# Performance work log

Measured on AMD Instinct MI355X. Metric: run time of the kernel, lower is better.

Reference implementation:

```python
import math
import jax, jax.numpy as jnp
import numpy as np

EPS = 1e-5

def _ln(x, g, b, axes):
    # LayerNormalization4D / 4DCF: mean/var (unbiased=False) over `axes`
    mu = x.mean(axis=axes, keepdims=True)
    var = ((x - mu) ** 2).mean(axis=axes, keepdims=True)
    return (x - mu) / jnp.sqrt(var + EPS) * g + b

def _prelu(x, a):
    return jnp.where(x >= 0, x, a * x)

def _unfold(x, ks, hs):
    # x: [N, C, Q] -> [N, L, C*ks]; patch layout (c, k) matches F.unfold
    N, C, Qd = x.shape
    L = (Qd - ks) // hs + 1
    idx = jnp.arange(L) * hs
    p = x[:, :, idx[:, None] + jnp.arange(ks)]  # [N, C, L, ks]
    return p.transpose(0, 2, 1, 3).reshape(N, L, C * ks)

def _lstm_dir(xs, Wi, Wh, bi, bh, H):
    # xs: [N, L, Cin]; torch gate order i, f, g, o
    xg = jnp.einsum('nlc,gc->nlg', xs, Wi) + bi + bh  # [N, L, 4H]
    def step(carry, gt):
        h, c = carry
        g = gt + h @ Wh.T
        i, f, gg, o = jnp.split(g, 4, axis=-1)
        c = jax.nn.sigmoid(f) * c + jax.nn.sigmoid(i) * jnp.tanh(gg)
        h = jax.nn.sigmoid(o) * jnp.tanh(c)
        return (h, c), h
    N = xs.shape[0]
    z = jnp.zeros((N, H), xs.dtype)
    _, hs = jax.lax.scan(step, (z, z), jnp.swapaxes(xg, 0, 1))
    return jnp.swapaxes(hs, 0, 1)

def _bilstm(x, wih, whh, bih, bhh):
    H = whh.shape[-1]
    f = _lstm_dir(x, wih[0], whh[0], bih[0], bhh[0], H)
    bk = _lstm_dir(x[:, ::-1], wih[1], whh[1], bih[1], bhh[1], H)[:, ::-1]
    return jnp.concatenate([f, bk], axis=-1)

def _convT1d(x, w, b):
    # x: [N, I, L]; w: [I, O, K] (torch ConvTranspose1d layout); stride 1
    K = w.shape[2]
    w2 = jnp.transpose(w, (1, 0, 2))[:, :, ::-1]
    y = jax.lax.conv_general_dilated(x, w2, (1,), [(K - 1, K - 1)],
                                     dimension_numbers=('NCH', 'OIH', 'NCH'))
    return y + b[None, :, None]

def _forward(x, mouth, intra_g, intra_b, intra_wih, intra_whh, intra_bih, intra_bhh,
             intra_lw, intra_lb, inter_g, inter_b, inter_wih, inter_whh, inter_bih,
             inter_bhh, inter_lw, inter_lb, qw, qb, qa, qg, qbe, kw, kb, ka, kg, kbe,
             vw, vb, va, vg, vbe, pw, pb, pa, pg, pbe):
    emb_ks, emb_hs = 4, 1
    B, C, oT, oQ = x.shape
    T = math.ceil((oT - emb_ks) / emb_hs) * emb_hs + emb_ks
    Qd = math.ceil((oQ - emb_ks) / emb_hs) * emb_hs + emb_ks
    x = jnp.pad(x, ((0, 0), (0, 0), (0, T - oT), (0, Qd - oQ)))
    inp = x
    # ---- intra (biLSTM along freq axis) ----
    h = _ln(inp, intra_g[None, :, None, None], intra_b[None, :, None, None], (1,))
    h = h.transpose(0, 2, 1, 3).reshape(B * T, C, Qd)
    h = _unfold(h, emb_ks, emb_hs)                          # [B*T, L, C*ks]
    h = _bilstm(h, intra_wih, intra_whh, intra_bih, intra_bhh)
    h = _convT1d(h.transpose(0, 2, 1), intra_lw, intra_lb)  # [B*T, C, Qd]
    intra = h.reshape(B, T, C, Qd).transpose(0, 2, 1, 3) + inp
    # ---- inter (biLSTM along time axis) ----
    h = _ln(intra, inter_g[None, :, None, None], inter_b[None, :, None, None], (1,))
    h = h.transpose(0, 3, 1, 2).reshape(B * Qd, C, T)
    h = _unfold(h, emb_ks, emb_hs)
    h = _bilstm(h, inter_wih, inter_whh, inter_bih, inter_bhh)
    h = _convT1d(h.transpose(0, 2, 1), inter_lw, inter_lb)  # [B*Qd, C, T]
    inter = h.reshape(B, Qd, C, T).transpose(0, 2, 3, 1) + intra
    inter = inter[..., :oT, :oQ]                             # [B, C, oT, oQ]
    # ---- multi-head full self-attention over time (conv1x1 QKV per head) ----
    NH = qw.shape[0]
    def qkv(w, b_, a_, g_, be_):
        y = jnp.einsum('bctf,hec->hbetf', inter, w) + b_[:, None, :, None, None]
        y = _prelu(y, a_[:, None, None, None, None])
        return _ln(y, g_[:, None, :, None, :], be_[:, None, :, None, :], (2, 4))
    Qh = qkv(qw, qb, qa, qg, qbe)   # [H, B, E, T, F]
    Kh = qkv(kw, kb, ka, kg, kbe)
    Vh = qkv(vw, vb, va, vg, vbe)   # [H, B, D, T, F]
    E = Qh.shape[2]; D = Vh.shape[2]; F = oQ
    q2 = Qh.transpose(0, 1, 3, 2, 4).reshape(NH, B, oT, E * F)
    k2 = Kh.transpose(0, 1, 3, 2, 4).reshape(NH, B, oT, E * F)
    v2 = Vh.transpose(0, 1, 3, 2, 4).reshape(NH, B, oT, D * F)
    scale = 1.0 / jnp.sqrt(jnp.asarray(E * F, x.dtype))
    attn = jax.nn.softmax(jnp.einsum('hbte,hbse->hbts', q2, k2) * scale, axis=-1)
    o = jnp.einsum('hbts,hbsd->hbtd', attn, v2).reshape(NH, B, oT, D, F)
    o = o.transpose(1, 0, 3, 2, 4).reshape(B, NH * D, oT, F)
    # ---- concat projection ----
    p = jnp.einsum('bctf,oc->botf', o, pw) + pb[None, :, None, None]
    p = _prelu(p, pa)
    p = _ln(p, pg[None, :, None, :], pbe[None, :, None, :], (1, 3))
    return p + inter

def setup_inputs() -> dict:
    key = jax.random.key(0)
    keys = iter(jax.random.split(key, 48))
    f32 = jnp.float32
    def nrm(shape, s=0.05):
        return jax.random.normal(next(keys), shape, f32) * s
    B, C, T, F = 2, 48, 512, 65
    K, H, NH, E = 4, 192, 4, 8
    Cin = C * K
    D = C // NH
    return {
        'x': jax.random.normal(next(keys), (B, C, T, F), f32),
        'mouth': jax.random.normal(next(keys), (B, 64), f32),
        'intra_g': jnp.ones((C,), f32), 'intra_b': jnp.zeros((C,), f32),
        'intra_wih': nrm((2, 4 * H, Cin)), 'intra_whh': nrm((2, 4 * H, H)),
        'intra_bih': nrm((2, 4 * H)), 'intra_bhh': nrm((2, 4 * H)),
        'intra_lw': nrm((2 * H, C, K)), 'intra_lb': nrm((C,)),
        'inter_g': jnp.ones((C,), f32), 'inter_b': jnp.zeros((C,), f32),
        'inter_wih': nrm((2, 4 * H, Cin)), 'inter_whh': nrm((2, 4 * H, H)),
        'inter_bih': nrm((2, 4 * H)), 'inter_bhh': nrm((2, 4 * H)),
        'inter_lw': nrm((2 * H, C, K)), 'inter_lb': nrm((C,)),
        'qw': nrm((NH, E, C)), 'qb': nrm((NH, E)), 'qa': 0.25 * jnp.ones((NH,), f32),
        'qg': jnp.ones((NH, E, F), f32), 'qbe': jnp.zeros((NH, E, F), f32),
        'kw': nrm((NH, E, C)), 'kb': nrm((NH, E)), 'ka': 0.25 * jnp.ones((NH,), f32),
        'kg': jnp.ones((NH, E, F), f32), 'kbe': jnp.zeros((NH, E, F), f32),
        'vw': nrm((NH, D, C)), 'vb': nrm((NH, D)), 'va': 0.25 * jnp.ones((NH,), f32),
        'vg': jnp.ones((NH, D, F), f32), 'vbe': jnp.zeros((NH, D, F), f32),
        'pw': nrm((C, C)), 'pb': nrm((C,)), 'pa': jnp.float32(0.25),
        'pg': jnp.ones((C, F), f32), 'pbe': jnp.zeros((C, F), f32),
    }

def reference(x, mouth, intra_g, intra_b, intra_wih, intra_whh, intra_bih, intra_bhh,
              intra_lw, intra_lb, inter_g, inter_b, inter_wih, inter_whh, inter_bih,
              inter_bhh, inter_lw, inter_lb, qw, qb, qa, qg, qbe, kw, kb, ka, kg, kbe,
              vw, vb, va, vg, vbe, pw, pb, pa, pg, pbe):
    return _forward(x, mouth, intra_g, intra_b, intra_wih, intra_whh, intra_bih,
                    intra_bhh, intra_lw, intra_lb, inter_g, inter_b, inter_wih,
                    inter_whh, inter_bih, inter_bhh, inter_lw, inter_lb, qw, qb, qa,
                    qg, qbe, kw, kb, ka, kg, kbe, vw, vb, va, vg, vbe, pw, pb, pa,
                    pg, pbe)
```

## Files before the change

### kernel.cpp

```cpp
#include <hip/hip_runtime.h>
#include <hip/hip_bf16.h>

typedef __bf16 bf16x8 __attribute__((ext_vector_type(8)));
typedef unsigned short u16x8 __attribute__((ext_vector_type(8)));
typedef float f32x4 __attribute__((ext_vector_type(4)));

#define DEV static __device__ __forceinline__

DEV unsigned short f2bf(float f){
  __hip_bfloat16 h = __float2bfloat16(f);
  return __builtin_bit_cast(unsigned short, h);
}
DEV float b2f(unsigned short u){
  return __bfloat162float(__builtin_bit_cast(__hip_bfloat16, u));
}
DEV float sig2(float xs){
  return __builtin_amdgcn_rcpf(1.0f + __builtin_amdgcn_exp2f(-xs));
}
DEV float tanh2s(float xs){
  return 1.0f - 2.0f*__builtin_amdgcn_rcpf(__builtin_amdgcn_exp2f(xs + xs) + 1.0f);
}
DEV float tanh_n(float x){
  return 1.0f - 2.0f*__builtin_amdgcn_rcpf(__builtin_amdgcn_exp2f(x * 2.885390082f) + 1.0f);
}
DEV void lds_barrier(){
  asm volatile("s_waitcnt lgkmcnt(0)\ns_barrier" ::: "memory");
}


__global__ void zero16(uint4* p, size_t n){
  size_t i = (size_t)blockIdx.x*blockDim.x + threadIdx.x;
  size_t st = (size_t)gridDim.x*blockDim.x;
  uint4 z = make_uint4(0u,0u,0u,0u);
  for (; i < n; i += st) p[i] = z;
}

__global__ void zero_pads(unsigned short* hs, int NSEQ, int Qrows, int L){
  int i = blockIdx.x*256 + threadIdx.x;
  int total = NSEQ*6*384;
  if (i < total){
    int t = i/(6*384); int rem = i - t*(6*384);
    int r = rem/384, c = rem - r*384;
    int row = r < 3 ? r : L + r;
    hs[((size_t)t*Qrows + row)*384 + c] = 0;
  }
}

__global__ void cast_bf(const float* __restrict__ s, unsigned short* __restrict__ d, int n, float scale){
  int i = blockIdx.x*256 + threadIdx.x;
  if (i < n) d[i] = f2bf(s[i]*scale);
}

__global__ void cast_wi(const float* __restrict__ s, unsigned short* __restrict__ d, float scale){
  int i = blockIdx.x*256 + threadIdx.x;
  if (i < 294912){
    int dn = i/192, k = i - dn*192;
    int c = k >> 2, kk = k & 3;
    d[(size_t)dn*192 + kk*48 + c] = f2bf(s[i]*scale);
  }
}

__global__ void bias_comb(const float* __restrict__ a, const float* __restrict__ b,
                          float* __restrict__ d, int n, float scale){
  int i = blockIdx.x*256 + threadIdx.x;
  if (i < n) d[i] = (a[i] + b[i])*scale;
}

__global__ void lwt_build(const float* __restrict__ lw, unsigned short* __restrict__ lwt){
  int i = blockIdx.x*256 + threadIdx.x;
  if (i < 384*48*4){
    int m = i / 192; int rest = i - m*192; int c = rest >> 2; int k = rest & 3;
    lwt[(size_t)c*1536 + k*384 + m] = f2bf(lw[i]);
  }
}

__global__ __launch_bounds__(256) void ln_unf_intra(
    const float* __restrict__ in, const float* __restrict__ g,
    const float* __restrict__ be, unsigned short* __restrict__ unf)
{
  int bt = blockIdx.x; int b = bt >> 9, t = bt & 511;
  __shared__ float v[48][66];
  __shared__ float mu[65], rs[65];
  __shared__ float g_l[48], b_l[48];
  const float* base = in + (size_t)b*(48*512*65) + (size_t)t*65;
  for (int i = threadIdx.x; i < 48*65; i += 256){
    int c = i/65, q = i - c*65;
    v[c][q] = base[(size_t)c*(512*65) + q];
  }
  if (threadIdx.x < 48){ g_l[threadIdx.x] = g[threadIdx.x]; b_l[threadIdx.x] = be[threadIdx.x]; }
  __syncthreads();
  if (threadIdx.x < 65){
    int q = threadIdx.x; float s=0.f, s2=0.f;
    #pragma unroll
    for (int c = 0; c < 48; c++){ float x = v[c][q]; s += x; s2 += x*x; }
    float m = s*(1.0f/48.0f);
    mu[q] = m; rs[q] = rsqrtf(s2*(1.0f/48.0f) - m*m + 1e-5f);
  }
  __syncthreads();
  unsigned short* orow = unf + (size_t)(b*512 + t)*62*192;
  for (int idx = threadIdx.x; idx < 62*24; idx += 256){
    int l = idx/24, jg = idx - l*24;
    int kk = jg/6, c0 = (jg - kk*6)*8;
    int q = l + kk;
    ushort4 p0, p1;
    float mq = mu[q], rq = rs[q];
    p0.x = f2bf((v[c0+0][q]-mq)*rq*g_l[c0+0] + b_l[c0+0]);
    p0.y = f2bf((v[c0+1][q]-mq)*rq*g_l[c0+1] + b_l[c0+1]);
    p0.z = f2bf((v[c0+2][q]-mq)*rq*g_l[c0+2] + b_l[c0+2]);
    p0.w = f2bf((v[c0+3][q]-mq)*rq*g_l[c0+3] + b_l[c0+3]);
    p1.x = f2bf((v[c0+4][q]-mq)*rq*g_l[c0+4] + b_l[c0+4]);
    p1.y = f2bf((v[c0+5][q]-mq)*rq*g_l[c0+5] + b_l[c0+5]);
    p1.z = f2bf((v[c0+6][q]-mq)*rq*g_l[c0+6] + b_l[c0+6]);
    p1.w = f2bf((v[c0+7][q]-mq)*rq*g_l[c0+7] + b_l[c0+7]);
    *(ushort4*)(orow + (size_t)l*192 + kk*48 + c0) = p0;
    *(ushort4*)(orow + (size_t)l*192 + kk*48 + c0 + 4) = p1;
  }
}

__global__ __launch_bounds__(256) void ln_unf_inter(
    const float* __restrict__ in, const float* __restrict__ g,
    const float* __restrict__ be, unsigned short* __restrict__ unf)
{
  int bt = blockIdx.x; int b = bt >> 9, t = bt & 511;
  __shared__ float v[48][66];
  __shared__ float mu[65], rs[65];
  __shared__ float g_l[48], b_l[48];
  const float* base = in + (size_t)b*(48*512*65) + (size_t)t*65;
  for (int i = threadIdx.x; i < 48*65; i += 256){
    int c = i/65, q = i - c*65;
    v[c][q] = base[(size_t)c*(512*65) + q];
  }
  if (threadIdx.x < 48){ g_l[threadIdx.x] = g[threadIdx.x]; b_l[threadIdx.x] = be[threadIdx.x]; }
  __syncthreads();
  if (threadIdx.x < 65){
    int q = threadIdx.x; float s=0.f, s2=0.f;
    #pragma unroll
    for (int c = 0; c < 48; c++){ float x = v[c][q]; s += x; s2 += x*x; }
    float m = s*(1.0f/48.0f);
    mu[q] = m; rs[q] = rsqrtf(s2*(1.0f/48.0f) - m*m + 1e-5f);
  }
  __syncthreads();
  for (int idx = threadIdx.x; idx < 4*65*6; idx += 256){
    int s = idx/390;
    int rem = idx - s*390;
    int q = rem/6, c0 = (rem - q*6)*8;
    int l = t - 3 + s, kk = 3 - s;
    if (l < 0 || l > 508) continue;
    float mq = mu[q], rq = rs[q];
    ushort4 p0, p1;
    p0.x = f2bf((v[c0+0][q]-mq)*rq*g_l[c0+0] + b_l[c0+0]);
    p0.y = f2bf((v[c0+1][q]-mq)*rq*g_l[c0+1] + b_l[c0+1]);
    p0.z = f2bf((v[c0+2][q]-mq)*rq*g_l[c0+2] + b_l[c0+2]);
    p0.w = f2bf((v[c0+3][q]-mq)*rq*g_l[c0+3] + b_l[c0+3]);
    p1.x = f2bf((v[c0+4][q]-mq)*rq*g_l[c0+4] + b_l[c0+4]);
    p1.y = f2bf((v[c0+5][q]-mq)*rq*g_l[c0+5] + b_l[c0+5]);
    p1.z = f2bf((v[c0+6][q]-mq)*rq*g_l[c0+6] + b_l[c0+6]);
    p1.w = f2bf((v[c0+7][q]-mq)*rq*g_l[c0+7] + b_l[c0+7]);
    size_t addr = ((size_t)(b*65+q)*509 + l)*192 + kk*48 + c0;
    *(ushort4*)(unf + addr) = p0;
    *(ushort4*)(unf + addr + 4) = p1;
  }
}

__global__ __launch_bounds__(256) void gemm_xg(
    const unsigned short* __restrict__ unf, const unsigned short* __restrict__ wib,
    const float* __restrict__ bias, unsigned short* __restrict__ xg,
    int NSEQ, int TW, int win0, int L, int nvalid)
{
  const int d = blockIdx.z;
  const int lane = threadIdx.x & 63, wave = threadIdx.x >> 6;
  const int kg = lane >> 4, lr = lane & 15;
  const int nslb = TW >> 3;
  const int sb  = blockIdx.x / nslb;
  const int slb = blockIdx.x - sb*nslb;
  const int nbase = blockIdx.y*64;
  const unsigned short* Bp = wib + (size_t)d*768*192;

  const unsigned short* abase[2];
  #pragma unroll
  for (int mt = 0; mt < 2; mt++){
    int sl = slb*8 + wave*2 + mt;
    int s = win0 + sl;
    int l = d ? (L-1-s) : s;
    l = l < 0 ? 0 : (l > L-1 ? L-1 : l);
    int seq = sb*16 + lr;
    seq = seq < nvalid ? seq : nvalid-1;
    abase[mt] = unf + ((size_t)seq*L + l)*192;
  }

  f32x4 acc[2][4] = {};
  #pragma unroll
  for (int kt = 0; kt < 6; kt++){
    int k0 = kt*32 + kg*8;
    bf16x8 a0 = *(const bf16x8*)(abase[0] + k0);
    bf16x8 a1 = *(const bf16x8*)(abase[1] + k0);
    #pragma unroll
    for (int nt = 0; nt < 4; nt++){
      int n = nbase + nt*16 + lr;
      bf16x8 bfr = *(const bf16x8*)(Bp + (size_t)n*192 + k0);
      acc[0][nt] = __builtin_amdgcn_mfma_f32_16x16x32_bf16(a0, bfr, acc[0][nt], 0,0,0);
      acc[1][nt] = __builtin_amdgcn_mfma_f32_16x16x32_bf16(a1, bfr, acc[1][nt], 0,0,0);
    }
  }
  #pragma unroll
  for (int mt = 0; mt < 2; mt++){
    int sl = slb*8 + wave*2 + mt;
    size_t rowb = (((size_t)d*(NSEQ>>4) + sb)*TW + sl)*768;
    #pragma unroll
    for (int nt = 0; nt < 4; nt++){
      int n = nbase + nt*16 + lr;
      float bs = bias[d*768 + n];
      ushort4 pk;
      pk.x = f2bf(acc[mt][nt][0] + bs);
      pk.y = f2bf(acc[mt][nt][1] + bs);
      pk.z = f2bf(acc[mt][nt][2] + bs);
      pk.w = f2bf(acc[mt][nt][3] + bs);
      *(ushort4*)(xg + (rowb + n)*16 + kg*4) = pk;
    }
  }
}

__global__ __launch_bounds__(768, 3) void fused_rec_xg(
    const unsigned short* __restrict__ xgA,
    const unsigned short* __restrict__ whb,
    unsigned short* __restrict__ hs,
    float* __restrict__ state,
    const unsigned short* __restrict__ unf,
    const unsigned short* __restrict__ wib,
    const float* __restrict__ bias,
    unsigned short* __restrict__ xgB,
    int NSEQ, int TW, int win0, int L, int Qrows, int nvalid, int steps,
    int NR, int NSBR, int NSLB, int win0x)
{
  const int tid = threadIdx.x;
  const int lane = tid & 63, w = tid >> 6;
  const int kg = lane >> 4, lr = lane & 15;

  __shared__ unsigned short h_lds[2][16][200];

  if ((int)blockIdx.x >= NR){
    int e = blockIdx.x - NR;
    int nb = e % 12; e /= 12;
    int slb = e % NSLB; e /= NSLB;
    int sb = e % NSBR; int d = e / NSBR;
    int sl = slb*12 + w;
    if (sl >= TW) return;
    int s = win0x + sl;
    int l = d ? (L-1-s) : s;
    l = l < 0 ? 0 : (l > L-1 ? L-1 : l);
    int seq = sb*16 + lr;
    seq = seq < nvalid ? seq : nvalid-1;
    const unsigned short* ab = unf + ((size_t)seq*L + l)*192;
    const unsigned short* Bp = wib + (size_t)d*768*192;
    const int nbase = nb*64;
    f32x4 acc[4] = {};
    #pragma unroll
    for (int kt = 0; kt < 6; kt++){
      int k0 = kt*32 + kg*8;
      bf16x8 a = *(const bf16x8*)(ab + k0);
      #pragma unroll
      for (int nt = 0; nt < 4; nt++){
        bf16x8 bfr = *(const bf16x8*)(Bp + (size_t)(nbase+nt*16+lr)*192 + k0);
        acc[nt] = __builtin_amdgcn_mfma_f32_16x16x32_bf16(a, bfr, acc[nt], 0,0,0);
      }
    }
    size_t rowb = (((size_t)d*NSBR + sb)*TW + sl)*768;
    #pragma unroll
    for (int nt = 0; nt < 4; nt++){
      int n = nbase + nt*16 + lr;
      float bs = bias[d*768 + n];
      ushort4 pk;
      pk.x = f2bf(acc[nt][0] + bs);
      pk.y = f2bf(acc[nt][1] + bs);
      pk.z = f2bf(acc[nt][2] + bs);
      pk.w = f2bf(acc[nt][3] + bs);
      *(ushort4*)(xgB + (rowb + n)*16 + kg*4) = pk;
    }
    return;
  }

  const int d = blockIdx.x / NSBR;
  const int sbx = blockIdx.x - d*NSBR;
  const int seq0 = sbx * 16;
  const int col = w*16 + lr;

  bf16x8 whf[4][6];
  #pragma unroll
  for (int g = 0; g < 4; g++){
    const unsigned short* wrow = whb + ((size_t)d*768 + g*192 + col)*192;
    #pragma unroll
    for (int kt = 0; kt < 6; kt++)
      whf[g][kt] = *(const bf16x8*)(wrow + kt*32 + kg*8);
  }

  float c_reg[4];
  unsigned short* hsp[4];
  bool val[4];
  const int l0 = d ? (L-1-win0) : win0;
  const ptrdiff_t ldelta = d ? -384 : 384;
  #pragma unroll
  for (int r = 0; r < 4; r++){
    int m = kg*4 + r;
    const float* st = state + (((size_t)d*NSEQ + seq0 + m)*2)*192;
    h_lds[0][m][col] = f2bf(st[col]);
    c_reg[r] = st[192 + col];
    val[r] = (seq0 + m) < nvalid;
    hsp[r] = hs + ((size_t)(seq0+m)*Qrows + (l0+3))*384 + d*192 + col;
  }
  lds_barrier();

  const unsigned short* xq0 = xgA + ((((size_t)d*NSBR + sbx)*TW)*768)*16
                              + ((size_t)col)*16 + kg*4;
  const size_t SSTR = (size_t)768*16;

  uint2 pfA[4], pfB[4];
  {
    const unsigned short* p1 = xq0 + (steps > 1 ? SSTR : 0);
    #pragma unroll
    for (int g = 0; g < 4; g++){
      pfA[g] = *(const uint2*)(xq0 + (size_t)g*(192*16));
      pfB[g] = *(const uint2*)(p1  + (size_t)g*(192*16));
    }
  }

  int cur = 0;
  auto do_step = [&](uint2 (&pf)[4], int ss){
    f32x4 acc[4];
    #pragma unroll
    for (int g = 0; g < 4; g++){
      unsigned int lo = pf[g].x, hi = pf[g].y;
      acc[g][0] = b2f((unsigned short)(lo & 0xffffu));
      acc[g][1] = b2f((unsigned short)(lo >> 16));
      acc[g][2] = b2f((unsigned short)(hi & 0xffffu));
      acc[g][3] = b2f((unsigned short)(hi >> 16));
    }
    int nss = ss + 2; nss = nss > steps-1 ? steps-1 : nss;
    const unsigned short* np = xq0 + (size_t)nss*SSTR;
    #pragma unroll
    for (int g = 0; g < 4; g++)
      pf[g] = *(const uint2*)(np + (size_t)g*(192*16));
    #pragma unroll
    for (int kt = 0; kt < 6; kt++){
      bf16x8 a = *(const bf16x8*)(&h_lds[cur][lr][kt*32 + kg*8]);
      #pragma unroll
      for (int g = 0; g < 4; g++)
        acc[g] = __builtin_amdgcn_mfma_f32_16x16x32_bf16(a, whf[g][kt], acc[g], 0,0,0);
    }
    #pragma unroll
    for (int r = 0; r < 4; r++){
      float gi = sig2(acc[0][r]);
      float gf = sig2(acc[1][r]);
      float gg = tanh2s(acc[2][r]);
      float go = sig2(acc[3][r]);
      float c = gf*c_reg[r] + gi*gg;
      c_reg[r] = c;
      float h = go*tanh_n(c);
      unsigned short hb = f2bf(h);
      h_lds[cur^1][kg*4 + r][col] = hb;
      if (val[r]) *hsp[r] = hb;
      hsp[r] += ldelta;
    }
    lds_barrier();
    cur ^= 1;
  };

  for (int ss = 0; ss < steps; ss += 2){
    do_step(pfA, ss);
    if (ss + 1 < steps) do_step(pfB, ss + 1);
  }

  #pragma unroll
  for (int r = 0; r < 4; r++){
    int m = kg*4 + r;
    float* st = state + (((size_t)d*NSEQ + seq0 + m)*2)*192;
    st[col] = b2f(h_lds[cur][m][col]);
    st[192 + col] = c_reg[r];
  }
}

template<int MODE>
__global__ __launch_bounds__(256) void gemm_convt(
    const unsigned short* __restrict__ hs, const unsigned short* __restrict__ lwt,
    const float* __restrict__ lb, const float* __restrict__ addsrc, float* __restrict__ dst)
{
  constexpr int Q  = MODE ? 512 : 65;
  const int lane = threadIdx.x & 63, wave = threadIdx.x >> 6;
  const int kg = lane >> 4, lr = lane & 15;
  const int R0 = blockIdx.x * 64;

  __shared__ union U {
    unsigned short a[27328];
    float c[64][52];
  } sm;

  const int HB0 = R0 + 3*(R0/Q);
  for (int idx = threadIdx.x; idx < 70*48; idx += 256){
    int j = idx/48, seg = idx - j*48;
    *(uint4*)&sm.a[(seg*71 + j)*8] = *(const uint4*)(hs + ((size_t)(HB0+j))*384 + seg*8);
  }
  __syncthreads();

  const int row = R0 + wave*16 + lr;
  const int an = row / Q;
  const int jb = row + 3*an - HB0;

  f32x4 acc[4] = {};
  for (int kt = 0; kt < 48; kt++){
    int k0 = kt*32 + kg*8;
    int tap = k0 / 384;
    int slot = (k0 >> 3) - tap*48;
    bf16x8 a = *(const bf16x8*)&sm.a[(slot*71 + jb + 3 - tap)*8];
    #pragma unroll
    for (int nt = 0; nt < 4; nt++){
      bf16x8 bfr = *(const bf16x8*)(lwt + (size_t)(nt*16+lr)*1536 + k0);
      acc[nt] = __builtin_amdgcn_mfma_f32_16x16x32_bf16(a, bfr, acc[nt], 0,0,0);
    }
  }

  if (MODE == 0){
    __syncthreads();
    #pragma unroll
    for (int nt = 0; nt < 3; nt++)
      #pragma unroll
      for (int r = 0; r < 4; r++)
        sm.c[wave*16 + kg*4 + r][nt*16 + lr] = acc[nt][r];
    __syncthreads();
    const int b = R0 >= 33280 ? 1 : 0;
    const size_t bb = (size_t)b*1597440;
    const int rb = R0 - b*33280;
    for (int idx = threadIdx.x; idx < 48*16; idx += 256){
      int n = idx >> 4, g = idx & 15;
      size_t off = bb + (size_t)n*33280 + rb + g*4;
      float4 av = *(const float4*)(addsrc + off);
      float lbn = lb[n];
      float4 o;
      o.x = sm.c[g*4+0][n] + lbn + av.x;
      o.y = sm.c[g*4+1][n] + lbn + av.y;
      o.z = sm.c[g*4+2][n] + lbn + av.z;
      o.w = sm.c[g*4+3][n] + lbn + av.w;
      *(float4*)(dst + off) = o;
    }
  } else {
    #pragma unroll
    for (int nt = 0; nt < 3; nt++){
      int n = nt*16 + lr;
      float lbn = lb[n];
      #pragma unroll
      for (int r = 0; r < 4; r++){
        int orow = R0 + wave*16 + kg*4 + r;
        int ns = orow >> 9, t = orow & 511;
        size_t off = (size_t)(ns/65)*1597440 + (size_t)n*33280 + (ns%65) + (size_t)t*65;
        dst[off] = acc[nt][r] + lbn + addsrc[off];
      }
    }
  }
}

__global__ __launch_bounds__(256) void gemm_rm(
    const unsigned short* __restrict__ A, const unsigned short* __restrict__ B, float* __restrict__ C,
    int lda, int ldb, int ldc, int KT, int nmax, long long strA, long long strB, long long strC)
{
  const int z = blockIdx.z;
  A += (size_t)z * strA; B += (size_t)z * strB; C += (size_t)z * strC;
  const int lane = threadIdx.x & 63, wave = threadIdx.x >> 6;
  const int kg = lane >> 4, lr = lane & 15;
  const int rowbase = blockIdx.x*128 + wave*32;
  const int nbase = blockIdx.y*64;
  f32x4 acc[2][4] = {};
  for (int kt = 0; kt < KT; kt++){
    int k0 = kt*32 + kg*8;
    bf16x8 a0 = *(const bf16x8*)(A + (size_t)(rowbase+lr)*lda + k0);
    bf16x8 a1 = *(const bf16x8*)(A + (size_t)(rowbase+16+lr)*lda + k0);
    #pragma unroll
    for (int nt = 0; nt < 4; nt++){
      bf16x8 bfr = *(const bf16x8*)(B + (size_t)(nbase+nt*16+lr)*ldb + k0);
      acc[0][nt] = __builtin_amdgcn_mfma_f32_16x16x32_bf16(a0, bfr, acc[0][nt], 0,0,0);
      acc[1][nt] = __builtin_amdgcn_mfma_f32_16x16x32_bf16(a1, bfr, acc[1][nt], 0,0,0);
    }
  }
  #pragma unroll
  for (int mt = 0; mt < 2; mt++)
  #pragma unroll
  for (int nt = 0; nt < 4; nt++)
  #pragma unroll
  for (int r = 0; r < 4; r++){
    int n = nbase + nt*16 + lr;
    if (n < nmax){
      int row = rowbase + mt*16 + kg*4 + r;
      C[(size_t)row*ldc + n] = acc[mt][nt][r];
    }
  }
}

__global__ __launch_bounds__(256) void qkv_k(
    const float* __restrict__ inter, const float* __restrict__ w, const float* __restrict__ bias,
    const float* __restrict__ alpha, const float* __restrict__ gam, const float* __restrict__ bet,
    unsigned short* __restrict__ out, int E, int mode)
{
  int t = blockIdx.x; int hb = blockIdx.y; int h = hb >> 1, b = hb & 1;
  __shared__ float in_l[48][66];
  __shared__ float w_l[12][48];
  __shared__ float y_l[780];
  __shared__ float rs1[4], rs2[4];
  const float* base = inter + (size_t)b*(48*512*65) + (size_t)t*65;
  for (int i = threadIdx.x; i < 48*65; i += 256){
    int c = i/65, f = i - c*65;
    in_l[c][f] = base[(size_t)c*(512*65) + f];
  }
  for (int i = threadIdx.x; i < E*48; i += 256) w_l[i/48][i - (i/48)*48] = w[(size_t)h*E*48 + i];
  __syncthreads();
  int nel = E*65;
  float a = alpha[h];
  float ps = 0.f, pq = 0.f;
  for (int i = threadIdx.x; i < nel; i += 256){
    int e = i/65, f = i - e*65;
    float s = bias[h*E + e];
    #pragma unroll
    for (int c = 0; c < 48; c++) s += w_l[e][c]*in_l[c][f];
    s = s >= 0.f ? s : a*s;
    y_l[i] = s; ps += s; pq += s*s;
  }
  #pragma unroll
  for (int o = 32; o; o >>= 1){ ps += __shfl_xor(ps, o); pq += __shfl_xor(pq, o); }
  if ((threadIdx.x & 63) == 0){ rs1[threadIdx.x>>6] = ps; rs2[threadIdx.x>>6] = pq; }
  __syncthreads();
  ps = rs1[0]+rs1[1]+rs1[2]+rs1[3]; pq = rs2[0]+rs2[1]+rs2[2]+rs2[3];
  float inv = 1.0f/(float)nel;
  float m = ps*inv; float rstd = rsqrtf(pq*inv - m*m + 1e-5f);
  for (int i = threadIdx.x; i < nel; i += 256){
    int e = i/65, f = i - e*65;
    float v = (y_l[i]-m)*rstd*gam[(size_t)(h*E+e)*65 + f] + bet[(size_t)(h*E+e)*65 + f];
    if (mode < 2) out[((size_t)hb*512 + t)*544 + i] = f2bf(v);
    else          out[((size_t)hb*832 + i)*512 + t] = f2bf(v);
  }
}

__global__ __launch_bounds__(256) void softmax_k(const float* __restrict__ S, unsigned short* __restrict__ P){
  size_t row = (size_t)blockIdx.y*512 + blockIdx.x;
  const float* s = S + row*512;
  int tid = threadIdx.x;
  float v0 = s[tid], v1 = s[tid+256];
  float m = fmaxf(v0, v1);
  #pragma unroll
  for (int o = 32; o; o >>= 1) m = fmaxf(m, __shfl_xor(m, o));
  __shared__ float r4[4], q4[4];
  if ((tid & 63) == 0) r4[tid>>6] = m;
  __syncthreads();
  m = fmaxf(fmaxf(r4[0], r4[1]), fmaxf(r4[2], r4[3]));
  const float sc = 0.04385290096535146f;
  float e0 = __expf((v0-m)*sc), e1 = __expf((v1-m)*sc);
  float su = e0 + e1;
  #pragma unroll
  for (int o = 32; o; o >>= 1) su += __shfl_xor(su, o);
  if ((tid & 63) == 0) q4[tid>>6] = su;
  __syncthreads();
  su = q4[0]+q4[1]+q4[2]+q4[3];
  float inv = __builtin_amdgcn_rcpf(su);
  unsigned short* p = P + row*512;
  p[tid] = f2bf(e0*inv); p[tid+256] = f2bf(e1*inv);
}

__global__ __launch_bounds__(256) void pout_k(
    const float* __restrict__ o, const float* __restrict__ pw, const float* __restrict__ pb,
    const float* __restrict__ pa, const float* __restrict__ pg, const float* __restrict__ pbe,
    const float* __restrict__ inter, float* __restrict__ out)
{
  int bt = blockIdx.x; int b = bt >> 9, t = bt & 511;
  __shared__ float o_l[48][66];
  __shared__ float pw_l[48][48];
  __shared__ float p_l[3120];
  __shared__ float rs1[4], rs2[4];
  for (int i = threadIdx.x; i < 48*65; i += 256){
    int c = i/65, f = i - c*65; int h = c/12, dd = c - h*12;
    o_l[c][f] = o[((size_t)(h*2+b)*512 + t)*780 + dd*65 + f];
  }
  for (int i = threadIdx.x; i < 48*48; i += 256) pw_l[i/48][i - (i/48)*48] = pw[i];
  __syncthreads();
  float a = pa[0];
  float ps = 0.f, pq = 0.f;
  for (int i = threadIdx.x; i < 3120; i += 256){
    int oc = i/65, f = i - oc*65;
    float s = pb[oc];
    #pragma unroll
    for (int c = 0; c < 48; c++) s += pw_l[oc][c]*o_l[c][f];
    s = s >= 0.f ? s : a*s;
    p_l[i] = s; ps += s; pq += s*s;
  }
  #pragma unroll
  for (int o2 = 32; o2; o2 >>= 1){ ps += __shfl_xor(ps, o2); pq += __shfl_xor(pq, o2); }
  if ((threadIdx.x & 63) == 0){ rs1[threadIdx.x>>6] = ps; rs2[threadIdx.x>>6] = pq; }
  __syncthreads();
  ps = rs1[0]+rs1[1]+rs1[2]+rs1[3]; pq = rs2[0]+rs2[1]+rs2[2]+rs2[3];
  float m = ps*(1.0f/3120.0f); float rstd = rsqrtf(pq*(1.0f/3120.0f) - m*m + 1e-5f);
  for (int i = threadIdx.x; i < 3120; i += 256){
    int oc = i/65, f = i - oc*65;
    size_t off = ((size_t)(b*48+oc)*512 + t)*65 + f;
    out[off] = (p_l[i]-m)*rstd*pg[i] + pbe[i] + inter[off];
  }
}


extern "C" void kernel_launch(void* const* d_in, const int* in_sizes, int n_in,
                              void* d_out, int out_size, void* d_ws, size_t ws_size,
                              hipStream_t stream)
{
  const float* x         = (const float*)d_in[0];
  const float* intra_g   = (const float*)d_in[2];
  const float* intra_b   = (const float*)d_in[3];
  const float* intra_wih = (const float*)d_in[4];
  const float* intra_whh = (const float*)d_in[5];
  const float* intra_bih = (const float*)d_in[6];
  const float* intra_bhh = (const float*)d_in[7];
  const float* intra_lw  = (const float*)d_in[8];
  const float* intra_lb  = (const float*)d_in[9];
  const float* inter_g   = (const float*)d_in[10];
  const float* inter_b   = (const float*)d_in[11];
  const float* inter_wih = (const float*)d_in[12];
  const float* inter_whh = (const float*)d_in[13];
  const float* inter_bih = (const float*)d_in[14];
  const float* inter_bhh = (const float*)d_in[15];
  const float* inter_lw  = (const float*)d_in[16];
  const float* inter_lb  = (const float*)d_in[17];
  const float* qw  = (const float*)d_in[18];
  const float* qb  = (const float*)d_in[19];
  const float* qa  = (const float*)d_in[20];
  const float* qg  = (const float*)d_in[21];
  const float* qbe = (const float*)d_in[22];
  const float* kw  = (const float*)d_in[23];
  const float* kb  = (const float*)d_in[24];
  const float* ka  = (const float*)d_in[25];
  const float* kgm = (const float*)d_in[26];
  const float* kbe = (const float*)d_in[27];
  const float* vw  = (const float*)d_in[28];
  const float* vb  = (const float*)d_in[29];
  const float* va  = (const float*)d_in[30];
  const float* vg  = (const float*)d_in[31];
  const float* vbe = (const float*)d_in[32];
  const float* pw  = (const float*)d_in[33];
  const float* pb  = (const float*)d_in[34];
  const float* pa  = (const float*)d_in[35];
  const float* pgm = (const float*)d_in[36];
  const float* pbe = (const float*)d_in[37];

  char* ws = (char*)d_ws;
  constexpr size_t WIB_INTRA = 0;
  constexpr size_t WHB_INTRA = 589824;
  constexpr size_t WIB_INTER = 1179648;
  constexpr size_t WHB_INTER = 1769472;
  constexpr size_t LWT_INTRA = 2359296;
  constexpr size_t LWT_INTER = 2555904;
  constexpr size_t BIAS_INTRA = 2752512;
  constexpr size_t BIAS_INTER = 2758656;
  constexpr size_t UNF   = 2764800;
  constexpr size_t INTER = 2764800;
  constexpr size_t STATE = 28311552;
  constexpr size_t HS    = 31457280;
  constexpr size_t INTRA = 84934656;
  constexpr size_t XG    = 97714176;
  constexpr size_t Q2B   = XG;
  constexpr size_t K2B   = XG + 4456448;
  constexpr size_t V2T   = XG + 8912896;
  constexpr size_t SCORES= XG + 15728640;
  constexpr size_t ATTNB = XG + 24117248;
  constexpr size_t OBUF  = XG + 28311552;

  auto U16 = [&](size_t off){ return (unsigned short*)(ws + off); };
  auto F32 = [&](size_t off){ return (float*)(ws + off); };

  const float LOG2E = 1.4426950408889634f;

  zero16<<<512,256,0,stream>>>((uint4*)(ws+LWT_INTRA), 393216/16);
  cast_wi<<<1152,256,0,stream>>>(intra_wih, U16(WIB_INTRA), LOG2E);
  cast_bf<<<1152,256,0,stream>>>(intra_whh, U16(WHB_INTRA), 294912, LOG2E);
  cast_wi<<<1152,256,0,stream>>>(inter_wih, U16(WIB_INTER), LOG2E);
  cast_bf<<<1152,256,0,stream>>>(inter_whh, U16(WHB_INTER), 294912, LOG2E);
  bias_comb<<<6,256,0,stream>>>(intra_bih, intra_bhh, F32(BIAS_INTRA), 1536, LOG2E);
  bias_comb<<<6,256,0,stream>>>(inter_bih, inter_bhh, F32(BIAS_INTER), 1536, LOG2E);
  lwt_build<<<288,256,0,stream>>>(intra_lw, U16(LWT_INTRA));
  lwt_build<<<288,256,0,stream>>>(inter_lw, U16(LWT_INTER));

  {
    unsigned short* xb[2] = { U16(XG), U16(XG + 25165824) };
    ln_unf_intra<<<1024,256,0,stream>>>(x, intra_g, intra_b, U16(UNF));
    zero_pads<<<9216,256,0,stream>>>(U16(HS), 1024, 68, 62);
    zero16<<<2048,256,0,stream>>>((uint4*)(ws+STATE), 3145728/16);
    gemm_xg<<<dim3(64,12,2),256,0,stream>>>(U16(UNF), U16(WIB_INTRA), F32(BIAS_INTRA), xb[0],
                                            1024, 8, 0, 62, 1024);
    for (int w = 0; w < 8; w++){
      int win0 = w*8;
      int steps = (62 - win0) < 8 ? (62 - win0) : 8;
      int nxg = (w < 7) ? 1536 : 0;
      fused_rec_xg<<<128 + nxg, 768, 0, stream>>>(
          xb[w&1], U16(WHB_INTRA), U16(HS), F32(STATE),
          U16(UNF), U16(WIB_INTRA), F32(BIAS_INTRA), xb[(w+1)&1],
          1024, 8, win0, 62, 68, 1024, steps,
          128, 64, 1, (w+1)*8);
    }
    gemm_convt<0><<<1040,256,0,stream>>>(U16(HS), U16(LWT_INTRA), intra_lb, x, F32(INTRA));
  }

  {
    unsigned short* xb[2] = { U16(XG), U16(XG + 14155776) };
    ln_unf_inter<<<1024,256,0,stream>>>(F32(INTRA), inter_g, inter_b, U16(UNF));
    zero_pads<<<1170,256,0,stream>>>(U16(HS), 130, 515, 509);
    zero16<<<2048,256,0,stream>>>((uint4*)(ws+STATE), 3145728/16);
    gemm_xg<<<dim3(36,12,2),256,0,stream>>>(U16(UNF), U16(WIB_INTER), F32(BIAS_INTER), xb[0],
                                            144, 32, 0, 509, 130);
    for (int w = 0; w < 16; w++){
      int win0 = w*32;
      int steps = (509 - win0) < 32 ? (509 - win0) : 32;
      int nxg = (w < 15) ? 648 : 0;
      fused_rec_xg<<<18 + nxg, 768, 0, stream>>>(
          xb[w&1], U16(WHB_INTER), U16(HS), F32(STATE),
          U16(UNF), U16(WIB_INTER), F32(BIAS_INTER), xb[(w+1)&1],
          144, 32, win0, 509, 515, 130, steps,
          18, 9, 3, (w+1)*32);
    }
    gemm_convt<1><<<1040,256,0,stream>>>(U16(HS), U16(LWT_INTER), inter_lb, F32(INTRA), F32(INTER));
  }

  zero16<<<2048,256,0,stream>>>((uint4*)(ws+Q2B), 15728640/16);
  qkv_k<<<dim3(512,8),256,0,stream>>>(F32(INTER), qw, qb, qa, qg, qbe, U16(Q2B), 8, 0);
  qkv_k<<<dim3(512,8),256,0,stream>>>(F32(INTER), kw, kb, ka, kgm, kbe, U16(K2B), 8, 1);
  qkv_k<<<dim3(512,8),256,0,stream>>>(F32(INTER), vw, vb, va, vg, vbe, U16(V2T), 12, 2);
  gemm_rm<<<dim3(4,8,8),256,0,stream>>>(U16(Q2B), U16(K2B), F32(SCORES),
                                        544, 544, 512, 17, 512,
                                        (long long)512*544, (long long)512*544, (long long)512*512);
  softmax_k<<<dim3(512,8),256,0,stream>>>(F32(SCORES), U16(ATTNB));
  gemm_rm<<<dim3(4,13,8),256,0,stream>>>(U16(ATTNB), U16(V2T), F32(OBUF),
                                         512, 512, 780, 16, 780,
                                         (long long)512*512, (long long)832*512, (long long)512*780);
  pout_k<<<1024,256,0,stream>>>(F32(OBUF), pw, pb, pa, pgm, pbe, F32(INTER), (float*)d_out);
}
```

Before: 1.829 ms.

## Stage convT weights in LDS, widen convT blocks, and enlarge inter LSTM windows

The transposed-conv GEMM now preloads the whole re-laid-out bf16 weight matrix into shared memory and streams activation rows straight from global memory with register prefetch. It uses 128-row, 512-thread blocks and drops the padded fourth N-tile, which also removes the weight-zeroing launch. Separately, the inter-chunk LSTM recurrence uses 48-step windows instead of 32, so there are fewer fused recurrence launches. The costs are a larger xg double buffer, one block per CU from the large LDS footprint, and more uncoalesced global reads of activations.

```diff
diff --git a/kernel.cpp b/kernel.cpp
--- a/kernel.cpp
+++ b/kernel.cpp
@@ -66,11 +66,12 @@
   if (i < n) d[i] = (a[i] + b[i])*scale;
 }
 
-__global__ void lwt_build(const float* __restrict__ lw, unsigned short* __restrict__ lwt){
+__global__ void lwt_build(const float* __restrict__ lw, unsigned short* __restrict__ lwt2){
   int i = blockIdx.x*256 + threadIdx.x;
   if (i < 384*48*4){
     int m = i / 192; int rest = i - m*192; int c = rest >> 2; int k = rest & 3;
-    lwt[(size_t)c*1536 + k*384 + m] = f2bf(lw[i]);
+    int kap = k*384 + m;
+    lwt2[((size_t)(kap>>3)*48 + c)*8 + (kap&7)] = f2bf(lw[i]);
   }
 }
 
@@ -379,40 +380,48 @@
 }
 
 template<int MODE>
-__global__ __launch_bounds__(256) void gemm_convt(
-    const unsigned short* __restrict__ hs, const unsigned short* __restrict__ lwt,
+__global__ __launch_bounds__(512, 1) void gemm_convt(
+    const unsigned short* __restrict__ hs, const unsigned short* __restrict__ lwt2,
     const float* __restrict__ lb, const float* __restrict__ addsrc, float* __restrict__ dst)
 {
   constexpr int Q  = MODE ? 512 : 65;
   const int lane = threadIdx.x & 63, wave = threadIdx.x >> 6;
   const int kg = lane >> 4, lr = lane & 15;
-  const int R0 = blockIdx.x * 64;
-
-  __shared__ union U {
-    unsigned short a[27328];
-    float c[64][52];
+  const int R0 = blockIdx.x * 128;
+
+  __shared__ union __align__(16) U {
+    unsigned short b[192*48*8];
+    float c[128][53];
   } sm;
 
-  const int HB0 = R0 + 3*(R0/Q);
-  for (int idx = threadIdx.x; idx < 70*48; idx += 256){
-    int j = idx/48, seg = idx - j*48;
-    *(uint4*)&sm.a[(seg*71 + j)*8] = *(const uint4*)(hs + ((size_t)(HB0+j))*384 + seg*8);
-  }
+  for (int cidx = threadIdx.x; cidx < 9216; cidx += 512)
+    *(uint4*)&sm.b[(size_t)cidx*8] = *(const uint4*)(lwt2 + (size_t)cidx*8);
   __syncthreads();
 
   const int row = R0 + wave*16 + lr;
-  const int an = row / Q;
-  const int jb = row + 3*an - HB0;
-
-  f32x4 acc[4] = {};
+  const int an = row / Q, aq = row - an*Q;
+  const unsigned short* ab[4];
+  #pragma unroll
+  for (int tap = 0; tap < 4; tap++)
+    ab[tap] = hs + ((size_t)an*(Q+3) + aq + 3 - tap)*384 + kg*8;
+
+  bf16x8 pf0 = *(const bf16x8*)(ab[0]);
+  bf16x8 pf1 = *(const bf16x8*)(ab[0] + 32);
+  int ntap = 0, nm = 2;
+
+  f32x4 acc[3] = {};
   for (int kt = 0; kt < 48; kt++){
-    int k0 = kt*32 + kg*8;
-    int tap = k0 / 384;
-    int slot = (k0 >> 3) - tap*48;
-    bf16x8 a = *(const bf16x8*)&sm.a[(slot*71 + jb + 3 - tap)*8];
-    #pragma unroll
-    for (int nt = 0; nt < 4; nt++){
-      bf16x8 bfr = *(const bf16x8*)(lwt + (size_t)(nt*16+lr)*1536 + k0);
+    bf16x8 a = pf0;
+    pf0 = pf1;
+    if (kt < 46){
+      pf1 = *(const bf16x8*)(ab[ntap] + nm*32);
+      nm++;
+      if (nm == 12){ nm = 0; ntap++; }
+    }
+    const int bo = (kt*4 + kg)*48*8;
+    #pragma unroll
+    for (int nt = 0; nt < 3; nt++){
+      bf16x8 bfr = *(const bf16x8*)&sm.b[bo + (nt*16 + lr)*8];
       acc[nt] = __builtin_amdgcn_mfma_f32_16x16x32_bf16(a, bfr, acc[nt], 0,0,0);
     }
   }
@@ -428,8 +437,8 @@
     const int b = R0 >= 33280 ? 1 : 0;
     const size_t bb = (size_t)b*1597440;
     const int rb = R0 - b*33280;
-    for (int idx = threadIdx.x; idx < 48*16; idx += 256){
-      int n = idx >> 4, g = idx & 15;
+    for (int idx = threadIdx.x; idx < 48*32; idx += 512){
+      int n = idx >> 5, g = idx & 31;
       size_t off = bb + (size_t)n*33280 + rb + g*4;
       float4 av = *(const float4*)(addsrc + off);
       float lbn = lb[n];
@@ -669,7 +678,6 @@
 
   const float LOG2E = 1.4426950408889634f;
 
-  zero16<<<512,256,0,stream>>>((uint4*)(ws+LWT_INTRA), 393216/16);
   cast_wi<<<1152,256,0,stream>>>(intra_wih, U16(WIB_INTRA), LOG2E);
   cast_bf<<<1152,256,0,stream>>>(intra_whh, U16(WHB_INTRA), 294912, LOG2E);
   cast_wi<<<1152,256,0,stream>>>(inter_wih, U16(WIB_INTER), LOG2E);
@@ -696,27 +704,27 @@
           1024, 8, win0, 62, 68, 1024, steps,
           128, 64, 1, (w+1)*8);
     }
-    gemm_convt<0><<<1040,256,0,stream>>>(U16(HS), U16(LWT_INTRA), intra_lb, x, F32(INTRA));
+    gemm_convt<0><<<520,512,0,stream>>>(U16(HS), U16(LWT_INTRA), intra_lb, x, F32(INTRA));
   }
 
   {
-    unsigned short* xb[2] = { U16(XG), U16(XG + 14155776) };
+    unsigned short* xb[2] = { U16(XG), U16(XG + 21233664) };
     ln_unf_inter<<<1024,256,0,stream>>>(F32(INTRA), inter_g, inter_b, U16(UNF));
     zero_pads<<<1170,256,0,stream>>>(U16(HS), 130, 515, 509);
     zero16<<<2048,256,0,stream>>>((uint4*)(ws+STATE), 3145728/16);
-    gemm_xg<<<dim3(36,12,2),256,0,stream>>>(U16(UNF), U16(WIB_INTER), F32(BIAS_INTER), xb[0],
-                                            144, 32, 0, 509, 130);
-    for (int w = 0; w < 16; w++){
-      int win0 = w*32;
-      int steps = (509 - win0) < 32 ? (509 - win0) : 32;
-      int nxg = (w < 15) ? 648 : 0;
+    gemm_xg<<<dim3(54,12,2),256,0,stream>>>(U16(UNF), U16(WIB_INTER), F32(BIAS_INTER), xb[0],
+                                            144, 48, 0, 509, 130);
+    for (int w = 0; w < 11; w++){
+      int win0 = w*48;
+      int steps = (509 - win0) < 48 ? (509 - win0) : 48;
+      int nxg = (w < 10) ? 864 : 0;
       fused_rec_xg<<<18 + nxg, 768, 0, stream>>>(
           xb[w&1], U16(WHB_INTER), U16(HS), F32(STATE),
           U16(UNF), U16(WIB_INTER), F32(BIAS_INTER), xb[(w+1)&1],
-          144, 32, win0, 509, 515, 130, steps,
-          18, 9, 3, (w+1)*32);
-    }
-    gemm_convt<1><<<1040,256,0,stream>>>(U16(HS), U16(LWT_INTER), inter_lb, F32(INTRA), F32(INTER));
+          144, 48, win0, 509, 515, 130, steps,
+          18, 9, 4, (w+1)*48);
+    }
+    gemm_convt<1><<<520,512,0,stream>>>(U16(HS), U16(LWT_INTER), inter_lb, F32(INTRA), F32(INTER));
   }
 
   zero16<<<2048,256,0,stream>>>((uint4*)(ws+Q2B), 15728640/16);
```

Result: faster. 1.651 ms (-9.7%).
